# Kernel tuning notes

Hardware: AMD Instinct MI355X
Metric: run time of the kernel (lower is better)

## Reference

```python
import jax, jax.numpy as jnp
import numpy as np

E = 1024   # embed_dim
H = 16     # num_heads
D = E // H # head_dim
M = 2048   # query length
N = 2048   # key/value length
B = 4      # batch
SCALE = 1.0 / float(np.sqrt(D))


def setup_inputs() -> dict:
    key = jax.random.key(0)
    ks = jax.random.split(key, 11)
    s = 0.02
    return {
        "query": jax.random.normal(ks[0], (M, B, E), jnp.float32),
        "key": jax.random.normal(ks[1], (N, B, E), jnp.float32),
        "value": jax.random.normal(ks[2], (N, B, E), jnp.float32),
        "Wq": jax.random.normal(ks[3], (E, E), jnp.float32) * s,
        "bq": jax.random.normal(ks[4], (E,), jnp.float32) * s,
        "Wk": jax.random.normal(ks[5], (E, E), jnp.float32) * s,
        "bk": jax.random.normal(ks[6], (E,), jnp.float32) * s,
        "Wv": jax.random.normal(ks[7], (E, E), jnp.float32) * s,
        "bv": jax.random.normal(ks[8], (E,), jnp.float32) * s,
        "Wo": jax.random.normal(ks[9], (E, E), jnp.float32) * s,
        "bo": jax.random.normal(ks[10], (E,), jnp.float32) * s,
    }


def reference(query, key, value, Wq, bq, Wk, bk, Wv, bv, Wo, bo):
    # batch_first=False: (M,B,E) -> (B,M,E)
    q = jnp.swapaxes(query, 0, 1)
    k = jnp.swapaxes(key, 0, 1)
    v = jnp.swapaxes(value, 0, 1)
    # projections (torch Linear: x @ W^T + b; here W stored as (in,out))
    q = (q @ Wq + bq).reshape(B, M, H, D)
    k = (k @ Wk + bk).reshape(B, N, H, D)
    v = (v @ Wv + bv).reshape(B, N, H, D)
    # per-head attention, vectorized over heads (same math as the Python loop)
    logits = jnp.einsum("bmhd,bnhd->bhmn", q, k) * SCALE
    attn = jax.nn.softmax(logits, axis=-1)
    out = jnp.einsum("bhmn,bnhd->bmhd", attn, v).reshape(B, M, E)
    out = out @ Wo + bo
    # back to (M,B,E)
    return jnp.swapaxes(out, 0, 1)
```

## Files before the change

kernel.cpp:

```cpp
#include <hip/hip_runtime.h>

typedef unsigned short u16;
typedef unsigned int u32;
typedef __bf16 bf16x8 __attribute__((ext_vector_type(8)));
typedef float f32x4 __attribute__((ext_vector_type(4)));
typedef float f32x16 __attribute__((ext_vector_type(16)));
typedef unsigned short u16x8 __attribute__((ext_vector_type(8)));
typedef unsigned short u16x4 __attribute__((ext_vector_type(4)));

#define LOG2E 1.44269504088896f

__device__ __forceinline__ float fast_exp2(float x) {
#if __has_builtin(__builtin_amdgcn_exp2f)
  return __builtin_amdgcn_exp2f(x);
#else
  return exp2f(x);
#endif
}

__device__ __forceinline__ u16 f2bf(float x) {
  union { __bf16 b; u16 u; } c;
  c.b = (__bf16)x;
  return c.u;
}

__device__ __forceinline__ u32 cvtpk_bf16(float lo_, float hi_) {
  u32 r;
  asm("v_cvt_pk_bf16_f32 %0, %1, %2" : "=v"(r) : "v"(lo_), "v"(hi_));
  return r;
}

__device__ __forceinline__ void permswap32(u32& a, u32& b) {
  asm volatile("v_permlane32_swap_b32 %0, %1" : "+v"(a), "+v"(b));
}

__device__ __forceinline__ void gload_lds16(const void* g, void* l) {
  __builtin_amdgcn_global_load_lds(
      (__attribute__((address_space(1))) void*)(g),
      (__attribute__((address_space(3))) void*)(l), 16, 0, 0);
}

__device__ __forceinline__ int swz_off(int row, int col) {
  return row * 64 + ((((col >> 3) ^ (row ^ (row >> 3))) & 7) << 3) + (col & 7);
}

__global__ __launch_bounds__(256) void transpose_cvt4(
    const float* __restrict__ Wq, const float* __restrict__ Wk,
    const float* __restrict__ Wv, const float* __restrict__ Wo,
    u16* __restrict__ Wqt, u16* __restrict__ Wkt,
    u16* __restrict__ Wvt, u16* __restrict__ Wot) {
  const int E = 1024;
  const float* W = blockIdx.z == 0 ? Wq : blockIdx.z == 1 ? Wk
                   : blockIdx.z == 2 ? Wv : Wo;
  u16* Wt = blockIdx.z == 0 ? Wqt : blockIdx.z == 1 ? Wkt
            : blockIdx.z == 2 ? Wvt : Wot;
  __shared__ float tile[32][33];
  int tx = threadIdx.x & 31, ty = threadIdx.x >> 5;
  int bx = blockIdx.x * 32, by = blockIdx.y * 32;
  #pragma unroll
  for (int i = 0; i < 32; i += 8)
    tile[ty + i][tx] = W[(size_t)(by + ty + i) * E + bx + tx];
  __syncthreads();
  #pragma unroll
  for (int i = 0; i < 32; i += 8)
    Wt[(size_t)(bx + ty + i) * E + by + tx] = f2bf(tile[tx][ty + i]);
}

__global__ __launch_bounds__(256) void proj_qkv(
    const float* __restrict__ Xq, const float* __restrict__ Xk,
    const float* __restrict__ Xv,
    const u16* __restrict__ Wqt, const u16* __restrict__ Wkt,
    const u16* __restrict__ Wvt,
    const float* __restrict__ bq, const float* __restrict__ bk,
    const float* __restrict__ bv,
    u16* __restrict__ Qp, u16* __restrict__ Kp, u16* __restrict__ Vp,
    float qscale)
{
  constexpr int K = 1024, N = 1024;
  const float* A; const u16* Bt; const float* bias; u16* C; float oscale;
  if (blockIdx.z == 0)      { A = Xq; Bt = Wqt; bias = bq; C = Qp; oscale = qscale; }
  else if (blockIdx.z == 1) { A = Xk; Bt = Wkt; bias = bk; C = Kp; oscale = 1.f; }
  else                      { A = Xv; Bt = Wvt; bias = bv; C = Vp; oscale = 1.f; }

  __shared__ u16 As[128 * 64];
  __shared__ u16 Bs[128 * 64];
  const int tid = threadIdx.x;
  const int w = tid >> 6;
  const int lane = tid & 63;
  const int lo = lane & 15, hi = lane >> 4;
  const int brow = blockIdx.x * 128;
  const int bcol = blockIdx.y * 128;
  const int wr = (w >> 1) * 64;
  const int wc = (w & 1) * 64;
  const int rowt = tid >> 3;
  const int ko = (tid & 7) * 8;
  const int pc = tid & 7;

  f32x4 acc[4][4] = {};

  for (int k0 = 0; k0 < K; k0 += 64) {
    __syncthreads();
    #pragma unroll
    for (int i = 0; i < 4; i++) {
      int row = i * 32 + rowt;
      int lc = pc ^ ((row ^ (row >> 3)) & 7);
      gload_lds16(Bt + (size_t)(bcol + row) * K + k0 + lc * 8,
                  (void*)(Bs + (size_t)(i * 256 + w * 64) * 8));
    }
    #pragma unroll
    for (int i = 0; i < 4; i++) {
      const float* Ap = A + (size_t)(brow + i * 32 + rowt) * K + k0 + ko;
      float4 v0 = *(const float4*)Ap;
      float4 v1 = *(const float4*)(Ap + 4);
      u16x8 ab;
      ab[0] = f2bf(v0.x); ab[1] = f2bf(v0.y); ab[2] = f2bf(v0.z); ab[3] = f2bf(v0.w);
      ab[4] = f2bf(v1.x); ab[5] = f2bf(v1.y); ab[6] = f2bf(v1.z); ab[7] = f2bf(v1.w);
      *(u16x8*)(As + swz_off(i * 32 + rowt, ko)) = ab;
    }
    __syncthreads();

    __builtin_amdgcn_s_setprio(1);
    #pragma unroll
    for (int kk = 0; kk < 2; kk++) {
      bf16x8 af[4], bfr[4];
      #pragma unroll
      for (int mi = 0; mi < 4; mi++)
        af[mi] = *(const bf16x8*)(As + swz_off(wr + mi * 16 + lo, kk * 32 + hi * 8));
      #pragma unroll
      for (int ni = 0; ni < 4; ni++)
        bfr[ni] = *(const bf16x8*)(Bs + swz_off(wc + ni * 16 + lo, kk * 32 + hi * 8));
      #pragma unroll
      for (int mi = 0; mi < 4; mi++)
        #pragma unroll
        for (int ni = 0; ni < 4; ni++)
          acc[mi][ni] = __builtin_amdgcn_mfma_f32_16x16x32_bf16(
              af[mi], bfr[ni], acc[mi][ni], 0, 0, 0);
    }
    __builtin_amdgcn_s_setprio(0);
  }

  #pragma unroll
  for (int mi = 0; mi < 4; mi++)
    #pragma unroll
    for (int ni = 0; ni < 4; ni++) {
      int row = brow + wr + mi * 16 + hi * 4;
      int col = bcol + wc + ni * 16 + lo;
      float bv = bias[col];
      #pragma unroll
      for (int r = 0; r < 4; r++) {
        float v = (acc[mi][ni][r] + bv) * oscale;
        C[(size_t)(row + r) * N + col] = f2bf(v);
      }
    }
}

__global__ __launch_bounds__(256) void gemm_out(
    const u16* __restrict__ A, const u16* __restrict__ Bt,
    const float* __restrict__ bias, float* __restrict__ C)
{
  constexpr int K = 1024, N = 1024;
  __shared__ u16 As[128 * 64];
  __shared__ u16 Bs[128 * 64];
  const int tid = threadIdx.x;
  const int w = tid >> 6;
  const int lane = tid & 63;
  const int lo = lane & 15, hi = lane >> 4;
  const int brow = blockIdx.x * 128;
  const int bcol = blockIdx.y * 128;
  const int wr = (w >> 1) * 64;
  const int wc = (w & 1) * 64;
  const int rowt = tid >> 3;
  const int pc = tid & 7;

  f32x4 acc[4][4] = {};

  for (int k0 = 0; k0 < K; k0 += 64) {
    __syncthreads();
    #pragma unroll
    for (int i = 0; i < 4; i++) {
      int row = i * 32 + rowt;
      int lc = pc ^ ((row ^ (row >> 3)) & 7);
      gload_lds16(A + (size_t)(brow + row) * K + k0 + lc * 8,
                  (void*)(As + (size_t)(i * 256 + w * 64) * 8));
      gload_lds16(Bt + (size_t)(bcol + row) * K + k0 + lc * 8,
                  (void*)(Bs + (size_t)(i * 256 + w * 64) * 8));
    }
    __syncthreads();
    __builtin_amdgcn_s_setprio(1);
    #pragma unroll
    for (int kk = 0; kk < 2; kk++) {
      bf16x8 af[4], bfr[4];
      #pragma unroll
      for (int mi = 0; mi < 4; mi++)
        af[mi] = *(const bf16x8*)(As + swz_off(wr + mi * 16 + lo, kk * 32 + hi * 8));
      #pragma unroll
      for (int ni = 0; ni < 4; ni++)
        bfr[ni] = *(const bf16x8*)(Bs + swz_off(wc + ni * 16 + lo, kk * 32 + hi * 8));
      #pragma unroll
      for (int mi = 0; mi < 4; mi++)
        #pragma unroll
        for (int ni = 0; ni < 4; ni++)
          acc[mi][ni] = __builtin_amdgcn_mfma_f32_16x16x32_bf16(
              af[mi], bfr[ni], acc[mi][ni], 0, 0, 0);
    }
    __builtin_amdgcn_s_setprio(0);
  }

  #pragma unroll
  for (int mi = 0; mi < 4; mi++)
    #pragma unroll
    for (int ni = 0; ni < 4; ni++) {
      int row = brow + wr + mi * 16 + hi * 4;
      int col = bcol + wc + ni * 16 + lo;
      float bv = bias[col];
      #pragma unroll
      for (int r = 0; r < 4; r++)
        C[(size_t)(row + r) * N + col] = acc[mi][ni][r] + bv;
    }
}

__global__ __launch_bounds__(256) void attn_kernel(
    const u16* __restrict__ Qp, const u16* __restrict__ Kp,
    const u16* __restrict__ Vp, u16* __restrict__ O)
{
  constexpr int Bb = 4, E = 1024, Nn = 2048;
  constexpr int NT = Nn / 64;
  __shared__ u16 Ks[2][64 * 64];
  __shared__ u16 Vt[2][64 * 64];

  const int tid = threadIdx.x;
  const int lane = tid & 63;
  const int w = tid >> 6;
  const int l31 = lane & 31;
  const int hi5 = lane >> 5;

  const int wg = blockIdx.x;
  const int swz = (wg & 7) * 128 + (wg >> 3);
  const int b_ = swz >> 8;
  const int h = (swz >> 4) & 15;
  const int mbase = (swz & 15) * 128 + w * 32;
  const int m = mbase + l31;

  bf16x8 q[4];
  {
    const u16* qrow = Qp + (size_t)(m * Bb + b_) * E + h * 64;
    #pragma unroll
    for (int kb = 0; kb < 4; kb++)
      q[kb] = *(const bf16x8*)(qrow + kb * 16 + hi5 * 8);
  }

  f32x16 oacc[2] = {};
  float lrun = 0.f;

  const int nrK = tid >> 3;
  const int q8K = (tid & 7) * 8;
  const int dq = (tid & 15) * 4;
  const int nq = (tid >> 4) * 4;
  const size_t rstride = (size_t)Bb * E;
  const size_t KSTEP = 64 * rstride;
  const u16* kpt = Kp + (size_t)nrK * rstride + (size_t)b_ * E + h * 64 + q8K;
  const u16* vpt = Vp + (size_t)nq * rstride + (size_t)b_ * E + h * 64 + dq;

  u16x8 kreg[2];
  u16x4 vreg[4];
  kreg[0] = *(const u16x8*)(kpt);
  kreg[1] = *(const u16x8*)(kpt + 32 * rstride);
  #pragma unroll
  for (int j = 0; j < 4; j++)
    vreg[j] = *(const u16x4*)(vpt + j * rstride);
  kpt += KSTEP; vpt += KSTEP;

  int it = 0;
  for (int t = 0; t < NT; t++, it ^= 1) {
    #pragma unroll
    for (int i = 0; i < 2; i++)
      *(u16x8*)(&Ks[it][swz_off(i * 32 + nrK, q8K)]) = kreg[i];
    #pragma unroll
    for (int jw = 0; jw < 4; jw++) {
      u16x4 colv;
      #pragma unroll
      for (int j = 0; j < 4; j++) colv[j] = vreg[j][jw];
      *(u16x4*)(&Vt[it][swz_off(dq + jw, nq)]) = colv;
    }
    __syncthreads();
    if (t < NT - 1) {
      kreg[0] = *(const u16x8*)(kpt);
      kreg[1] = *(const u16x8*)(kpt + 32 * rstride);
      #pragma unroll
      for (int j = 0; j < 4; j++)
        vreg[j] = *(const u16x4*)(vpt + j * rstride);
      kpt += KSTEP; vpt += KSTEP;
    }
    const u16* ksp = &Ks[it][0];
    const u16* vtp = &Vt[it][0];

    f32x16 st[2];
    __builtin_amdgcn_s_setprio(1);
    #pragma unroll
    for (int sb = 0; sb < 2; sb++) {
      f32x16 tacc = {};
      #pragma unroll
      for (int kb = 0; kb < 4; kb++) {
        bf16x8 kf = *(const bf16x8*)(ksp + swz_off(sb * 32 + l31, kb * 16 + hi5 * 8));
        tacc = __builtin_amdgcn_mfma_f32_32x32x16_bf16(kf, q[kb], tacc, 0, 0, 0);
      }
      st[sb] = tacc;
    }
    __builtin_amdgcn_s_setprio(0);

    u32 pk[2][8];
    float ra = 0.f, rb = 0.f, rc = 0.f, rd = 0.f;
    #pragma unroll
    for (int sb = 0; sb < 2; sb++) {
      #pragma unroll
      for (int j = 0; j < 8; j++) {
        float p0 = fast_exp2(st[sb][2 * j]);
        float p1 = fast_exp2(st[sb][2 * j + 1]);
        if (j & 1) { ra += p0; rb += p1; } else { rc += p0; rd += p1; }
        pk[sb][j] = cvtpk_bf16(p0, p1);
      }
    }
    lrun += (ra + rb) + (rc + rd);

    bf16x8 pb[4];
    #pragma unroll
    for (int kb = 0; kb < 4; kb++) {
      int sb = kb >> 1, c = kb & 1;
      u32 a0 = pk[sb][4 * c + 0], b0 = pk[sb][4 * c + 2];
      u32 a1 = pk[sb][4 * c + 1], b1 = pk[sb][4 * c + 3];
      permswap32(a0, b0);
      permswap32(a1, b1);
      union { u32 d[4]; bf16x8 v; } u;
      u.d[0] = a0; u.d[1] = a1; u.d[2] = b0; u.d[3] = b1;
      pb[kb] = u.v;
    }

    __builtin_amdgcn_s_setprio(1);
    #pragma unroll
    for (int dsb = 0; dsb < 2; dsb++) {
      #pragma unroll
      for (int kb = 0; kb < 4; kb++) {
        bf16x8 vf = *(const bf16x8*)(vtp + swz_off(dsb * 32 + l31, kb * 16 + hi5 * 8));
        oacc[dsb] = __builtin_amdgcn_mfma_f32_32x32x16_bf16(vf, pb[kb], oacc[dsb], 0, 0, 0);
      }
    }
    __builtin_amdgcn_s_setprio(0);
  }

  float l = lrun + __shfl_xor(lrun, 32);
  float inv = 1.f / l;
  u16* orow = O + (size_t)(m * Bb + b_) * E + h * 64;
  #pragma unroll
  for (int dsb = 0; dsb < 2; dsb++) {
    #pragma unroll
    for (int qd = 0; qd < 4; qd++) {
      u16x4 o;
      #pragma unroll
      for (int t = 0; t < 4; t++) o[t] = f2bf(oacc[dsb][qd * 4 + t] * inv);
      *(u16x4*)(orow + dsb * 32 + qd * 8 + hi5 * 4) = o;
    }
  }
}

extern "C" void kernel_launch(void* const* d_in, const int* in_sizes, int n_in,
                              void* d_out, int out_size, void* d_ws, size_t ws_size,
                              hipStream_t stream) {
  const float* query = (const float*)d_in[0];
  const float* key   = (const float*)d_in[1];
  const float* value = (const float*)d_in[2];
  const float* Wq = (const float*)d_in[3];
  const float* bq = (const float*)d_in[4];
  const float* Wk = (const float*)d_in[5];
  const float* bk = (const float*)d_in[6];
  const float* Wv = (const float*)d_in[7];
  const float* bv = (const float*)d_in[8];
  const float* Wo = (const float*)d_in[9];
  const float* bo = (const float*)d_in[10];
  float* out = (float*)d_out;

  const float QSCALE = 0.125f * LOG2E;

  const size_t XE = (size_t)2048 * 4 * 1024;
  const size_t WE = (size_t)1024 * 1024;
  u16* ws  = (u16*)d_ws;
  u16* Qp  = ws;
  u16* Kp  = Qp + XE;
  u16* Vp  = Kp + XE;
  u16* Ob  = Vp + XE;
  u16* Wqt = Ob + XE;
  u16* Wkt = Wqt + WE;
  u16* Wvt = Wkt + WE;
  u16* Wot = Wvt + WE;

  dim3 blk(256);
  transpose_cvt4<<<dim3(32, 32, 4), blk, 0, stream>>>(
      Wq, Wk, Wv, Wo, Wqt, Wkt, Wvt, Wot);

  proj_qkv<<<dim3(64, 8, 3), blk, 0, stream>>>(
      query, key, value, Wqt, Wkt, Wvt, bq, bk, bv, Qp, Kp, Vp, QSCALE);

  attn_kernel<<<1024, blk, 0, stream>>>(Qp, Kp, Vp, Ob);

  gemm_out<<<dim3(64, 8), blk, 0, stream>>>(Ob, Wot, bo, out);
}
```

Before: 215.0 us.

## Pre-convert activations to bf16 and reuse one bf16 GEMM for projections

Replaces the fused QKV projection kernel, which converted fp32 activations to bf16 inside the GEMM tile loop, with a separate elementwise fp32-to-bf16 conversion pass per input followed by a templated bf16 GEMM that streams both operands into LDS via direct global-to-LDS loads. This halves the A-operand bytes read per tile and removes conversion ALU work from the GEMM inner loop. In exchange it adds three extra conversion kernels, an extra round trip through a scratch buffer, and serializes the three projections into six launches instead of one.

```diff
diff --git a/kernel.cpp b/kernel.cpp
--- a/kernel.cpp
+++ b/kernel.cpp
@@ -42,6 +42,17 @@
 
 __device__ __forceinline__ int swz_off(int row, int col) {
   return row * 64 + ((((col >> 3) ^ (row ^ (row >> 3))) & 7) << 3) + (col & 7);
+}
+
+__global__ __launch_bounds__(256) void cvt8(const float* __restrict__ in,
+                                            u16* __restrict__ out) {
+  int i = (blockIdx.x * 256 + threadIdx.x) * 8;
+  float4 v0 = *(const float4*)(in + i);
+  float4 v1 = *(const float4*)(in + i + 4);
+  u16x8 o;
+  o[0] = f2bf(v0.x); o[1] = f2bf(v0.y); o[2] = f2bf(v0.z); o[3] = f2bf(v0.w);
+  o[4] = f2bf(v1.x); o[5] = f2bf(v1.y); o[6] = f2bf(v1.z); o[7] = f2bf(v1.w);
+  *(u16x8*)(out + i) = o;
 }
 
 __global__ __launch_bounds__(256) void transpose_cvt4(
@@ -66,97 +77,10 @@
     Wt[(size_t)(bx + ty + i) * E + by + tx] = f2bf(tile[tx][ty + i]);
 }
 
-__global__ __launch_bounds__(256) void proj_qkv(
-    const float* __restrict__ Xq, const float* __restrict__ Xk,
-    const float* __restrict__ Xv,
-    const u16* __restrict__ Wqt, const u16* __restrict__ Wkt,
-    const u16* __restrict__ Wvt,
-    const float* __restrict__ bq, const float* __restrict__ bk,
-    const float* __restrict__ bv,
-    u16* __restrict__ Qp, u16* __restrict__ Kp, u16* __restrict__ Vp,
-    float qscale)
-{
-  constexpr int K = 1024, N = 1024;
-  const float* A; const u16* Bt; const float* bias; u16* C; float oscale;
-  if (blockIdx.z == 0)      { A = Xq; Bt = Wqt; bias = bq; C = Qp; oscale = qscale; }
-  else if (blockIdx.z == 1) { A = Xk; Bt = Wkt; bias = bk; C = Kp; oscale = 1.f; }
-  else                      { A = Xv; Bt = Wvt; bias = bv; C = Vp; oscale = 1.f; }
-
-  __shared__ u16 As[128 * 64];
-  __shared__ u16 Bs[128 * 64];
-  const int tid = threadIdx.x;
-  const int w = tid >> 6;
-  const int lane = tid & 63;
-  const int lo = lane & 15, hi = lane >> 4;
-  const int brow = blockIdx.x * 128;
-  const int bcol = blockIdx.y * 128;
-  const int wr = (w >> 1) * 64;
-  const int wc = (w & 1) * 64;
-  const int rowt = tid >> 3;
-  const int ko = (tid & 7) * 8;
-  const int pc = tid & 7;
-
-  f32x4 acc[4][4] = {};
-
-  for (int k0 = 0; k0 < K; k0 += 64) {
-    __syncthreads();
-    #pragma unroll
-    for (int i = 0; i < 4; i++) {
-      int row = i * 32 + rowt;
-      int lc = pc ^ ((row ^ (row >> 3)) & 7);
-      gload_lds16(Bt + (size_t)(bcol + row) * K + k0 + lc * 8,
-                  (void*)(Bs + (size_t)(i * 256 + w * 64) * 8));
-    }
-    #pragma unroll
-    for (int i = 0; i < 4; i++) {
-      const float* Ap = A + (size_t)(brow + i * 32 + rowt) * K + k0 + ko;
-      float4 v0 = *(const float4*)Ap;
-      float4 v1 = *(const float4*)(Ap + 4);
-      u16x8 ab;
-      ab[0] = f2bf(v0.x); ab[1] = f2bf(v0.y); ab[2] = f2bf(v0.z); ab[3] = f2bf(v0.w);
-      ab[4] = f2bf(v1.x); ab[5] = f2bf(v1.y); ab[6] = f2bf(v1.z); ab[7] = f2bf(v1.w);
-      *(u16x8*)(As + swz_off(i * 32 + rowt, ko)) = ab;
-    }
-    __syncthreads();
-
-    __builtin_amdgcn_s_setprio(1);
-    #pragma unroll
-    for (int kk = 0; kk < 2; kk++) {
-      bf16x8 af[4], bfr[4];
-      #pragma unroll
-      for (int mi = 0; mi < 4; mi++)
-        af[mi] = *(const bf16x8*)(As + swz_off(wr + mi * 16 + lo, kk * 32 + hi * 8));
-      #pragma unroll
-      for (int ni = 0; ni < 4; ni++)
-        bfr[ni] = *(const bf16x8*)(Bs + swz_off(wc + ni * 16 + lo, kk * 32 + hi * 8));
-      #pragma unroll
-      for (int mi = 0; mi < 4; mi++)
-        #pragma unroll
-        for (int ni = 0; ni < 4; ni++)
-          acc[mi][ni] = __builtin_amdgcn_mfma_f32_16x16x32_bf16(
-              af[mi], bfr[ni], acc[mi][ni], 0, 0, 0);
-    }
-    __builtin_amdgcn_s_setprio(0);
-  }
-
-  #pragma unroll
-  for (int mi = 0; mi < 4; mi++)
-    #pragma unroll
-    for (int ni = 0; ni < 4; ni++) {
-      int row = brow + wr + mi * 16 + hi * 4;
-      int col = bcol + wc + ni * 16 + lo;
-      float bv = bias[col];
-      #pragma unroll
-      for (int r = 0; r < 4; r++) {
-        float v = (acc[mi][ni][r] + bv) * oscale;
-        C[(size_t)(row + r) * N + col] = f2bf(v);
-      }
-    }
-}
-
-__global__ __launch_bounds__(256) void gemm_out(
+template <typename OutT>
+__global__ __launch_bounds__(256) void gemm_bt(
     const u16* __restrict__ A, const u16* __restrict__ Bt,
-    const float* __restrict__ bias, float* __restrict__ C)
+    const float* __restrict__ bias, OutT* __restrict__ C, float oscale)
 {
   constexpr int K = 1024, N = 1024;
   __shared__ u16 As[128 * 64];
@@ -214,8 +138,13 @@
       int col = bcol + wc + ni * 16 + lo;
       float bv = bias[col];
       #pragma unroll
-      for (int r = 0; r < 4; r++)
-        C[(size_t)(row + r) * N + col] = acc[mi][ni][r] + bv;
+      for (int r = 0; r < 4; r++) {
+        float v = (acc[mi][ni][r] + bv) * oscale;
+        if constexpr (sizeof(OutT) == 2)
+          C[(size_t)(row + r) * N + col] = (OutT)f2bf(v);
+        else
+          C[(size_t)(row + r) * N + col] = (OutT)v;
+      }
     }
 }
 
@@ -383,23 +312,31 @@
   const size_t XE = (size_t)2048 * 4 * 1024;
   const size_t WE = (size_t)1024 * 1024;
   u16* ws  = (u16*)d_ws;
-  u16* Qp  = ws;
+  u16* Xb  = ws;
+  u16* Qp  = Xb + XE;
   u16* Kp  = Qp + XE;
   u16* Vp  = Kp + XE;
-  u16* Ob  = Vp + XE;
-  u16* Wqt = Ob + XE;
+  u16* Wqt = Vp + XE;
   u16* Wkt = Wqt + WE;
   u16* Wvt = Wkt + WE;
   u16* Wot = Wvt + WE;
+  u16* Ob  = Xb;
 
   dim3 blk(256);
+  dim3 gg(64, 8);
+  const int ncvt = (int)(XE / 8 / 256);
+
   transpose_cvt4<<<dim3(32, 32, 4), blk, 0, stream>>>(
       Wq, Wk, Wv, Wo, Wqt, Wkt, Wvt, Wot);
 
-  proj_qkv<<<dim3(64, 8, 3), blk, 0, stream>>>(
-      query, key, value, Wqt, Wkt, Wvt, bq, bk, bv, Qp, Kp, Vp, QSCALE);
+  cvt8<<<ncvt, blk, 0, stream>>>(query, Xb);
+  gemm_bt<u16><<<gg, blk, 0, stream>>>(Xb, Wqt, bq, Qp, QSCALE);
+  cvt8<<<ncvt, blk, 0, stream>>>(key, Xb);
+  gemm_bt<u16><<<gg, blk, 0, stream>>>(Xb, Wkt, bk, Kp, 1.0f);
+  cvt8<<<ncvt, blk, 0, stream>>>(value, Xb);
+  gemm_bt<u16><<<gg, blk, 0, stream>>>(Xb, Wvt, bv, Vp, 1.0f);
 
   attn_kernel<<<1024, blk, 0, stream>>>(Qp, Kp, Vp, Ob);
 
-  gemm_out<<<dim3(64, 8), blk, 0, stream>>>(Ob, Wot, bo, out);
-}
+  gemm_bt<float><<<gg, blk, 0, stream>>>(Ob, Wot, bo, out, 1.0f);
+}
```

Result: slower. 221.6 us (+3.0%).

## Load K tiles directly to LDS and compute row sums via MFMA

Applied to the files above, without the earlier changes.

K tiles are now fetched with direct global-to-LDS loads, with the XOR swizzle applied on the source address, replacing the register staging and ds_write path. The V transpose is rebuilt with byte-permute instructions instead of per-element shuffles. The softmax row sum is accumulated by an extra MFMA against a ones vector, replacing the scalar adds and the final cross-lane shuffle. The aim is to cut VALU and LDS-write work in the inner loop at the cost of extra MFMA issue, and the row sum now uses bf16-rounded probabilities.

```diff
diff --git a/kernel.cpp b/kernel.cpp
--- a/kernel.cpp
+++ b/kernel.cpp
@@ -249,47 +249,70 @@
       q[kb] = *(const bf16x8*)(qrow + kb * 16 + hi5 * 8);
   }
 
+  bf16x8 ones;
+  {
+    union { u32 d[4]; bf16x8 v; } u;
+    u.d[0] = u.d[1] = u.d[2] = u.d[3] = 0x3F803F80u;
+    ones = u.v;
+  }
+
   f32x16 oacc[2] = {};
-  float lrun = 0.f;
+  f32x16 lacc = {};
 
   const int nrK = tid >> 3;
-  const int q8K = (tid & 7) * 8;
+  const int pcK = tid & 7;
   const int dq = (tid & 15) * 4;
   const int nq = (tid >> 4) * 4;
   const size_t rstride = (size_t)Bb * E;
-  const size_t KSTEP = 64 * rstride;
-  const u16* kpt = Kp + (size_t)nrK * rstride + (size_t)b_ * E + h * 64 + q8K;
+  const u16* kbase = Kp + (size_t)b_ * E + h * 64;
   const u16* vpt = Vp + (size_t)nq * rstride + (size_t)b_ * E + h * 64 + dq;
 
-  u16x8 kreg[2];
+  auto issueK = [&](int t, int buf) {
+    #pragma unroll
+    for (int i = 0; i < 2; i++) {
+      int row = i * 32 + nrK;
+      int lc = pcK ^ ((row ^ (row >> 3)) & 7);
+      gload_lds16(kbase + (size_t)(t * 64 + row) * rstride + lc * 8,
+                  (void*)(&Ks[buf][0] + (size_t)(i * 256 + w * 64) * 8));
+    }
+  };
+
   u16x4 vreg[4];
-  kreg[0] = *(const u16x8*)(kpt);
-  kreg[1] = *(const u16x8*)(kpt + 32 * rstride);
+  issueK(0, 0);
   #pragma unroll
   for (int j = 0; j < 4; j++)
-    vreg[j] = *(const u16x4*)(vpt + j * rstride);
-  kpt += KSTEP; vpt += KSTEP;
+    vreg[j] = *(const u16x4*)(vpt + (size_t)j * rstride);
 
   int it = 0;
   for (int t = 0; t < NT; t++, it ^= 1) {
-    #pragma unroll
-    for (int i = 0; i < 2; i++)
-      *(u16x8*)(&Ks[it][swz_off(i * 32 + nrK, q8K)]) = kreg[i];
-    #pragma unroll
-    for (int jw = 0; jw < 4; jw++) {
-      u16x4 colv;
-      #pragma unroll
-      for (int j = 0; j < 4; j++) colv[j] = vreg[j][jw];
-      *(u16x4*)(&Vt[it][swz_off(dq + jw, nq)]) = colv;
+    {
+      union U { u16x4 v; u32 d[2]; };
+      U u0, u1, u2, u3;
+      u0.v = vreg[0]; u1.v = vreg[1]; u2.v = vreg[2]; u3.v = vreg[3];
+      const u32 selA = 0x05040100u, selB = 0x07060302u;
+      u32 c[4][2];
+      c[0][0] = __builtin_amdgcn_perm(u1.d[0], u0.d[0], selA);
+      c[0][1] = __builtin_amdgcn_perm(u3.d[0], u2.d[0], selA);
+      c[1][0] = __builtin_amdgcn_perm(u1.d[0], u0.d[0], selB);
+      c[1][1] = __builtin_amdgcn_perm(u3.d[0], u2.d[0], selB);
+      c[2][0] = __builtin_amdgcn_perm(u1.d[1], u0.d[1], selA);
+      c[2][1] = __builtin_amdgcn_perm(u3.d[1], u2.d[1], selA);
+      c[3][0] = __builtin_amdgcn_perm(u1.d[1], u0.d[1], selB);
+      c[3][1] = __builtin_amdgcn_perm(u3.d[1], u2.d[1], selB);
+      #pragma unroll
+      for (int jw = 0; jw < 4; jw++) {
+        union { u32 d[2]; u16x4 v; } cv;
+        cv.d[0] = c[jw][0]; cv.d[1] = c[jw][1];
+        *(u16x4*)(&Vt[it][swz_off(dq + jw, nq)]) = cv.v;
+      }
     }
     __syncthreads();
-    if (t < NT - 1) {
-      kreg[0] = *(const u16x8*)(kpt);
-      kreg[1] = *(const u16x8*)(kpt + 32 * rstride);
+
+    if (t + 1 < NT) {
+      issueK(t + 1, it ^ 1);
       #pragma unroll
       for (int j = 0; j < 4; j++)
-        vreg[j] = *(const u16x4*)(vpt + j * rstride);
-      kpt += KSTEP; vpt += KSTEP;
+        vreg[j] = *(const u16x4*)(vpt + (size_t)((t + 1) * 64 + j) * rstride);
     }
     const u16* ksp = &Ks[it][0];
     const u16* vtp = &Vt[it][0];
@@ -309,18 +332,15 @@
     __builtin_amdgcn_s_setprio(0);
 
     u32 pk[2][8];
-    float ra = 0.f, rb = 0.f, rc = 0.f, rd = 0.f;
     #pragma unroll
     for (int sb = 0; sb < 2; sb++) {
       #pragma unroll
       for (int j = 0; j < 8; j++) {
         float p0 = fast_exp2(st[sb][2 * j]);
         float p1 = fast_exp2(st[sb][2 * j + 1]);
-        if (j & 1) { ra += p0; rb += p1; } else { rc += p0; rd += p1; }
         pk[sb][j] = cvtpk_bf16(p0, p1);
       }
     }
-    lrun += (ra + rb) + (rc + rd);
 
     bf16x8 pb[4];
     #pragma unroll
@@ -337,6 +357,9 @@
 
     __builtin_amdgcn_s_setprio(1);
     #pragma unroll
+    for (int kb = 0; kb < 4; kb++)
+      lacc = __builtin_amdgcn_mfma_f32_32x32x16_bf16(ones, pb[kb], lacc, 0, 0, 0);
+    #pragma unroll
     for (int dsb = 0; dsb < 2; dsb++) {
       #pragma unroll
       for (int kb = 0; kb < 4; kb++) {
@@ -347,8 +370,7 @@
     __builtin_amdgcn_s_setprio(0);
   }
 
-  float l = lrun + __shfl_xor(lrun, 32);
-  float inv = 1.f / l;
+  float inv = 1.f / lacc[0];
   u16* orow = O + (size_t)(m * Bb + b_) * E + h * 64;
   #pragma unroll
   for (int dsb = 0; dsb < 2; dsb++) {
```

Result: no change. 218.4 us (+1.6%).
